# Kernel optimization log

Measured on AMD Instinct MI355X. Metric: run time of the kernel, lower is better.

The kernel has to match this reference:

```python
import jax, jax.numpy as jnp
import numpy as np

N, E, G = 20000, 320000, 64
IN, HID, HEADS, EDGE_D, ACT = 128, 256, 4, 5, 8
NEG_SLOPE = 0.2


def setup_inputs() -> dict:
    key = jax.random.key(0)
    ks = jax.random.split(key, 24)
    g = lambda i, shape, scale=0.05: jax.random.normal(ks[i], shape, dtype=jnp.float32) * scale
    inp = {
        "x": jax.random.normal(ks[0], (N, IN), dtype=jnp.float32),
        "edge_index": jax.random.randint(ks[1], (2, E), 0, N, dtype=jnp.int64),
        "batch": jnp.sort(jax.random.randint(ks[2], (N,), 0, G, dtype=jnp.int64)),
        "edge_attr": jax.random.normal(ks[3], (E, EDGE_D), dtype=jnp.float32),
        # GATv2 layer 1: in->64 per head, 4 heads, concat -> 256
        "W1l": g(4, (IN, HID)), "W1r": g(5, (IN, HID)), "W1e": g(6, (EDGE_D, HID)),
        "att1": g(7, (HEADS, HID // HEADS)), "b1": jnp.zeros((HID,), jnp.float32),
        # GATv2 layer 2: 256->256, 1 head
        "W2l": g(8, (HID, HID)), "W2r": g(9, (HID, HID)), "W2e": g(10, (EDGE_D, HID)),
        "att2": g(11, (1, HID)), "b2": jnp.zeros((HID,), jnp.float32),
        # heads
        "Wp": g(12, (HID, ACT)), "bp": jnp.zeros((ACT,), jnp.float32),
        "Wv": g(13, (HID, 1)), "bv": jnp.zeros((1,), jnp.float32),
    }
    return inp


def gatv2_conv(x, src, dst, edge_attr, Wl, Wr, We, att, bias, heads, concat):
    # PyG GATv2Conv (share_weights=False, add_self_loops=False):
    #   x_l = lin_l(x) (source msg), x_r = lin_r(x) (target), e = lin_edge(edge_attr)
    #   score = att . leaky_relu(x_l[src] + x_r[dst] + e); segment-softmax over dst
    #   out[i] = sum_j alpha_ij * x_l[j]
    n = x.shape[0]
    c = Wl.shape[1] // heads
    xl = (x @ Wl).reshape(n, heads, c)
    xr = (x @ Wr).reshape(n, heads, c)
    e = (edge_attr @ We).reshape(-1, heads, c)
    m = jax.nn.leaky_relu(xl[src] + xr[dst] + e, NEG_SLOPE)      # [E, H, C]
    logit = jnp.einsum("ehc,hc->eh", m, att)                      # [E, H]
    lmax = jax.ops.segment_max(logit, dst, num_segments=n)        # [N, H]
    unnorm = jnp.exp(logit - lmax[dst])
    denom = jax.ops.segment_sum(unnorm, dst, num_segments=n)
    alpha = unnorm / (denom[dst] + 1e-16)                         # [E, H]
    out = jax.ops.segment_sum(alpha[:, :, None] * xl[src], dst, num_segments=n)  # [N,H,C]
    out = out.reshape(n, heads * c) if concat else out.mean(axis=1)
    return out + bias


def reference(x, edge_index, batch, edge_attr,
              W1l, W1r, W1e, att1, b1,
              W2l, W2r, W2e, att2, b2,
              Wp, bp, Wv, bv):
    src, dst = edge_index[0], edge_index[1]
    h = gatv2_conv(x, src, dst, edge_attr, W1l, W1r, W1e, att1, b1, HEADS, True)
    h = jax.nn.relu(h)  # dropout p=0.0 -> identity
    h = gatv2_conv(h, src, dst, edge_attr, W2l, W2r, W2e, att2, b2, 1, False)
    h = jax.nn.relu(h)
    # global mean pool over graphs
    sums = jax.ops.segment_sum(h, batch, num_segments=G)
    cnt = jax.ops.segment_sum(jnp.ones((h.shape[0],), h.dtype), batch, num_segments=G)
    g = sums / jnp.maximum(cnt, 1.0)[:, None]
    logits = g @ Wp + bp                 # [G, ACT]
    value = (g @ Wv + bv)[:, 0]          # [G]
    # deterministic outputs (sampling excluded): concat logits and value
    return jnp.concatenate([logits, value[:, None]], axis=-1)  # [G, ACT+1]
```

## Files before the change

### kernel.cpp

```cpp
#include <hip/hip_runtime.h>
#include <math.h>

#define NN 20000
#define NE 320000
#define NG 64
#define IND 128
#define HIDD 256
#define NH 4
#define ED 5
#define NACT 8
#define NEG 0.2f
#define MAXDEG 64

__global__ __launch_bounds__(256) void gemm64(const float* __restrict__ A,
    const float* __restrict__ B, float* __restrict__ C, int M, int K, int Ncol)
{
    const int BK = 32;
    __shared__ float As[32][68];
    __shared__ float Bs[32][64];
    int bm = blockIdx.x * 64, bn = blockIdx.y * 64;
    int tid = threadIdx.x;
    int tx = tid & 15, ty = tid >> 4;
    float acc[4][4] = {};
    for (int k0 = 0; k0 < K; k0 += BK) {
        for (int idx = tid; idx < 64 * BK; idx += 256) {
            int r = idx >> 5, c = idx & 31;
            int gr = bm + r;
            As[c][r] = (gr < M) ? A[(size_t)gr * K + k0 + c] : 0.f;
        }
        for (int idx = tid; idx < BK * 64; idx += 256) {
            int r = idx >> 6, c = idx & 63;
            Bs[r][c] = B[(size_t)(k0 + r) * Ncol + bn + c];
        }
        __syncthreads();
        #pragma unroll
        for (int k = 0; k < BK; ++k) {
            float4 a4 = *(const float4*)&As[k][ty * 4];
            float4 b4 = *(const float4*)&Bs[k][tx * 4];
            float a[4] = {a4.x, a4.y, a4.z, a4.w};
            float b[4] = {b4.x, b4.y, b4.z, b4.w};
            #pragma unroll
            for (int i = 0; i < 4; ++i)
                #pragma unroll
                for (int j = 0; j < 4; ++j)
                    acc[i][j] = fmaf(a[i], b[j], acc[i][j]);
        }
        __syncthreads();
    }
    #pragma unroll
    for (int i = 0; i < 4; ++i) {
        int r = bm + ty * 4 + i;
        if (r < M) {
            float4 v = {acc[i][0], acc[i][1], acc[i][2], acc[i][3]};
            *(float4*)&C[(size_t)r * Ncol + bn + tx * 4] = v;
        }
    }
}

__global__ __launch_bounds__(256) void build_slots(const int* __restrict__ dst,
    int* __restrict__ deg, int* __restrict__ slots)
{
    int e = blockIdx.x * 256 + threadIdx.x;
    if (e >= NE) return;
    int d = dst[e];
    int pos = atomicAdd(&deg[d], 1);
    if (pos < MAXDEG) slots[d * MAXDEG + pos] = e;
}

template <int HEADS_T>
__global__ __launch_bounds__(256) void fused_agg(
    const int* __restrict__ deg, const int* __restrict__ slots,
    const int* __restrict__ src, const float* __restrict__ eattr,
    const float* __restrict__ xl, const float* __restrict__ xr,
    const float* __restrict__ We, const float* __restrict__ attw,
    const float* __restrict__ bias, float* __restrict__ out)
{
    __shared__ float sWe[ED * HIDD];
    __shared__ float sAtt[HIDD];
    for (int i = threadIdx.x; i < ED * HIDD; i += 256) sWe[i] = We[i];
    for (int i = threadIdx.x; i < HIDD; i += 256) sAtt[i] = attw[i];
    __syncthreads();

    int wave = threadIdx.x >> 6, lane = threadIdx.x & 63;
    int n = blockIdx.x * 4 + wave;
    int dg = min(deg[n], MAXDEG);
    int c0 = lane * 4;

    float attr_[4], wer[ED][4];
    #pragma unroll
    for (int j = 0; j < 4; ++j) attr_[j] = sAtt[c0 + j];
    #pragma unroll
    for (int k = 0; k < ED; ++k)
        #pragma unroll
        for (int j = 0; j < 4; ++j) wer[k][j] = sWe[k * HIDD + c0 + j];

    float4 xr4 = *(const float4*)(xr + (size_t)n * HIDD + c0);
    float xra[4] = {xr4.x, xr4.y, xr4.z, xr4.w};

    float denom = 0.f;
    float acc[4] = {0.f, 0.f, 0.f, 0.f};

    const int* slotrow = slots + (size_t)n * MAXDEG;
    for (int i = 0; i < dg; ++i) {
        int e = slotrow[i];
        int s = src[e];
        float4 xl4 = *(const float4*)(xl + (size_t)s * HIDD + c0);
        float xla[4] = {xl4.x, xl4.y, xl4.z, xl4.w};
        float ea[ED];
        #pragma unroll
        for (int k = 0; k < ED; ++k) ea[k] = eattr[(size_t)e * ED + k];
        float partial = 0.f;
        #pragma unroll
        for (int j = 0; j < 4; ++j) {
            float ev = 0.f;
            #pragma unroll
            for (int k = 0; k < ED; ++k) ev = fmaf(ea[k], wer[k][j], ev);
            float m = xla[j] + xra[j] + ev;
            m = m > 0.f ? m : NEG * m;
            partial = fmaf(m, attr_[j], partial);
        }
        if (HEADS_T == 4) {
            #pragma unroll
            for (int off = 1; off < 16; off <<= 1)
                partial += __shfl_xor(partial, off, 64);
        } else {
            #pragma unroll
            for (int off = 1; off < 64; off <<= 1)
                partial += __shfl_xor(partial, off, 64);
        }
        float ex = expf(partial);
        denom += ex;
        #pragma unroll
        for (int j = 0; j < 4; ++j) acc[j] = fmaf(ex, xla[j], acc[j]);
    }
    float inv = 1.f / (denom + 1e-16f);
    float4 o;
    o.x = fmaxf(acc[0] * inv + bias[c0 + 0], 0.f);
    o.y = fmaxf(acc[1] * inv + bias[c0 + 1], 0.f);
    o.z = fmaxf(acc[2] * inv + bias[c0 + 2], 0.f);
    o.w = fmaxf(acc[3] * inv + bias[c0 + 3], 0.f);
    *(float4*)(out + (size_t)n * HIDD + c0) = o;
}

#define POOL_CHUNK 128
__global__ __launch_bounds__(256) void pool_kernel(
    const float* __restrict__ h, const int* __restrict__ batch,
    float* __restrict__ pool, float* __restrict__ cnt)
{
    int c = threadIdx.x;
    int start = blockIdx.x * POOL_CHUNK;
    int end = min(start + POOL_CHUNK, NN);
    if (start >= NN) return;
    float acc = 0.f;
    int cur = batch[start];
    int localCount = 0;
    for (int n = start; n < end; ++n) {
        int g = batch[n];
        if (g != cur) {
            atomicAdd(&pool[cur * HIDD + c], acc);
            if (c == 0) atomicAdd(&cnt[cur], (float)localCount);
            acc = 0.f; localCount = 0; cur = g;
        }
        acc += h[(size_t)n * HIDD + c];
        ++localCount;
    }
    atomicAdd(&pool[cur * HIDD + c], acc);
    if (c == 0) atomicAdd(&cnt[cur], (float)localCount);
}

__global__ __launch_bounds__(256) void head_kernel(
    const float* __restrict__ pool, const float* __restrict__ cnt,
    const float* __restrict__ Wp, const float* __restrict__ bp,
    const float* __restrict__ Wv, const float* __restrict__ bv,
    float* __restrict__ out)
{
    int g = blockIdx.x;
    int c = threadIdx.x;
    float gv = pool[g * HIDD + c] / fmaxf(cnt[g], 1.0f);
    __shared__ float red[256];
    for (int j = 0; j < NACT + 1; ++j) {
        float w = (j < NACT) ? Wp[c * NACT + j] : Wv[c];
        red[c] = gv * w;
        __syncthreads();
        for (int sl = 128; sl > 0; sl >>= 1) {
            if (c < sl) red[c] += red[c + sl];
            __syncthreads();
        }
        if (c == 0) out[g * (NACT + 1) + j] = red[0] + ((j < NACT) ? bp[j] : bv[0]);
        __syncthreads();
    }
}

extern "C" void kernel_launch(void* const* d_in, const int* in_sizes, int n_in,
                              void* d_out, int out_size, void* d_ws, size_t ws_size,
                              hipStream_t stream)
{
    const float* x    = (const float*)d_in[0];
    const int*   ei   = (const int*)d_in[1];
    const int*   batch= (const int*)d_in[2];
    const float* ea   = (const float*)d_in[3];
    const float* W1l  = (const float*)d_in[4];
    const float* W1r  = (const float*)d_in[5];
    const float* W1e  = (const float*)d_in[6];
    const float* att1 = (const float*)d_in[7];
    const float* b1   = (const float*)d_in[8];
    const float* W2l  = (const float*)d_in[9];
    const float* W2r  = (const float*)d_in[10];
    const float* W2e  = (const float*)d_in[11];
    const float* att2 = (const float*)d_in[12];
    const float* b2   = (const float*)d_in[13];
    const float* Wp   = (const float*)d_in[14];
    const float* bp   = (const float*)d_in[15];
    const float* Wv   = (const float*)d_in[16];
    const float* bv   = (const float*)d_in[17];
    const int* src = ei;
    const int* dst = ei + NE;
    float* out = (float*)d_out;

    float* ws = (float*)d_ws;
    size_t off = 0;
    float* A     = ws + off; off += (size_t)NN * HIDD;
    float* B     = ws + off; off += (size_t)NN * HIDD;
    float* C     = ws + off; off += (size_t)NN * HIDD;
    float* D     = ws + off; off += (size_t)NN * HIDD;
    float* pool  = ws + off; off += (size_t)NG * HIDD;
    float* cnt   = ws + off; off += NG;
    int*   deg   = (int*)(ws + off); off += NN;
    int*   slots = (int*)(ws + off); off += (size_t)NN * MAXDEG;

    hipMemsetAsync(pool, 0, (size_t)(NG * HIDD + NG + NN) * sizeof(float), stream);

    build_slots<<<(NE + 255) / 256, 256, 0, stream>>>(dst, deg, slots);

    dim3 ggrid((NN + 63) / 64, HIDD / 64);
    gemm64<<<ggrid, 256, 0, stream>>>(x, W1l, A, NN, IND, HIDD);
    gemm64<<<ggrid, 256, 0, stream>>>(x, W1r, B, NN, IND, HIDD);
    fused_agg<4><<<NN / 4, 256, 0, stream>>>(deg, slots, src, ea, A, B, W1e, att1, b1, C);

    gemm64<<<ggrid, 256, 0, stream>>>(C, W2l, A, NN, HIDD, HIDD);
    gemm64<<<ggrid, 256, 0, stream>>>(C, W2r, B, NN, HIDD, HIDD);
    fused_agg<1><<<NN / 4, 256, 0, stream>>>(deg, slots, src, ea, A, B, W2e, att2, b2, D);

    pool_kernel<<<(NN + POOL_CHUNK - 1) / POOL_CHUNK, 256, 0, stream>>>(D, batch, pool, cnt);
    head_kernel<<<NG, 256, 0, stream>>>(pool, cnt, Wp, bp, Wv, bv, out);
}
```

Measured before the change: 485.0 us.

## Enlarge GEMM tile to 128x64, vectorize loads, and batch left/right projections

Replaces the 64x64-tile GEMM with a 128x64 tile where each thread computes an 8x4 output block, which raises arithmetic intensity per shared-memory load. Global loads of A and B now use float4. The two projections (Wl and Wr) run in one launch via blockIdx.z, removing one launch per layer. The trade-off is more registers per thread and a padded 129-wide As array, whose strided transposed writes may cause bank conflicts.

```diff
diff --git a/kernel.cpp b/kernel.cpp
--- a/kernel.cpp
+++ b/kernel.cpp
@@ -12,35 +12,51 @@
 #define NEG 0.2f
 #define MAXDEG 64
 
-__global__ __launch_bounds__(256) void gemm64(const float* __restrict__ A,
-    const float* __restrict__ B, float* __restrict__ C, int M, int K, int Ncol)
-{
-    const int BK = 32;
-    __shared__ float As[32][68];
+__global__ __launch_bounds__(256, 4) void gemm128x64(
+    const float* __restrict__ A, const float* __restrict__ Bl,
+    const float* __restrict__ Br, float* __restrict__ Cl, float* __restrict__ Cr,
+    int M, int K, int Ncol)
+{
+    const float* B = blockIdx.z ? Br : Bl;
+    float*       C = blockIdx.z ? Cr : Cl;
+    __shared__ float As[32][129];
     __shared__ float Bs[32][64];
-    int bm = blockIdx.x * 64, bn = blockIdx.y * 64;
+    int bm = blockIdx.x * 128, bn = blockIdx.y * 64;
     int tid = threadIdx.x;
     int tx = tid & 15, ty = tid >> 4;
-    float acc[4][4] = {};
-    for (int k0 = 0; k0 < K; k0 += BK) {
-        for (int idx = tid; idx < 64 * BK; idx += 256) {
-            int r = idx >> 5, c = idx & 31;
+    float acc[8][4] = {};
+    for (int k0 = 0; k0 < K; k0 += 32) {
+        #pragma unroll
+        for (int t = 0; t < 4; ++t) {
+            int idx = tid + t * 256;
+            int r = idx >> 3;
+            int c4 = (idx & 7) * 4;
             int gr = bm + r;
-            As[c][r] = (gr < M) ? A[(size_t)gr * K + k0 + c] : 0.f;
-        }
-        for (int idx = tid; idx < BK * 64; idx += 256) {
-            int r = idx >> 6, c = idx & 63;
-            Bs[r][c] = B[(size_t)(k0 + r) * Ncol + bn + c];
-        }
-        __syncthreads();
-        #pragma unroll
-        for (int k = 0; k < BK; ++k) {
-            float4 a4 = *(const float4*)&As[k][ty * 4];
-            float4 b4 = *(const float4*)&Bs[k][tx * 4];
-            float a[4] = {a4.x, a4.y, a4.z, a4.w};
-            float b[4] = {b4.x, b4.y, b4.z, b4.w};
-            #pragma unroll
-            for (int i = 0; i < 4; ++i)
+            float4 v = {0.f, 0.f, 0.f, 0.f};
+            if (gr < M) v = *(const float4*)&A[(size_t)gr * K + k0 + c4];
+            As[c4 + 0][r] = v.x;
+            As[c4 + 1][r] = v.y;
+            As[c4 + 2][r] = v.z;
+            As[c4 + 3][r] = v.w;
+        }
+        #pragma unroll
+        for (int t = 0; t < 2; ++t) {
+            int idx = tid + t * 256;
+            int r = idx >> 4;
+            int c4 = (idx & 15) * 4;
+            float4 v = *(const float4*)&B[(size_t)(k0 + r) * Ncol + bn + c4];
+            *(float4*)&Bs[r][c4] = v;
+        }
+        __syncthreads();
+        #pragma unroll
+        for (int k = 0; k < 32; ++k) {
+            float4 a0 = *(const float4*)&As[k][ty * 8];
+            float4 a1 = *(const float4*)&As[k][ty * 8 + 4];
+            float4 b0 = *(const float4*)&Bs[k][tx * 4];
+            float a[8] = {a0.x, a0.y, a0.z, a0.w, a1.x, a1.y, a1.z, a1.w};
+            float b[4] = {b0.x, b0.y, b0.z, b0.w};
+            #pragma unroll
+            for (int i = 0; i < 8; ++i)
                 #pragma unroll
                 for (int j = 0; j < 4; ++j)
                     acc[i][j] = fmaf(a[i], b[j], acc[i][j]);
@@ -48,8 +64,8 @@
         __syncthreads();
     }
     #pragma unroll
-    for (int i = 0; i < 4; ++i) {
-        int r = bm + ty * 4 + i;
+    for (int i = 0; i < 8; ++i) {
+        int r = bm + ty * 8 + i;
         if (r < M) {
             float4 v = {acc[i][0], acc[i][1], acc[i][2], acc[i][3]};
             *(float4*)&C[(size_t)r * Ncol + bn + tx * 4] = v;
@@ -232,13 +248,11 @@
 
     build_slots<<<(NE + 255) / 256, 256, 0, stream>>>(dst, deg, slots);
 
-    dim3 ggrid((NN + 63) / 64, HIDD / 64);
-    gemm64<<<ggrid, 256, 0, stream>>>(x, W1l, A, NN, IND, HIDD);
-    gemm64<<<ggrid, 256, 0, stream>>>(x, W1r, B, NN, IND, HIDD);
+    dim3 g1((NN + 127) / 128, HIDD / 64, 2);
+    gemm128x64<<<g1, 256, 0, stream>>>(x, W1l, W1r, A, B, NN, IND, HIDD);
     fused_agg<4><<<NN / 4, 256, 0, stream>>>(deg, slots, src, ea, A, B, W1e, att1, b1, C);
 
-    gemm64<<<ggrid, 256, 0, stream>>>(C, W2l, A, NN, HIDD, HIDD);
-    gemm64<<<ggrid, 256, 0, stream>>>(C, W2r, B, NN, HIDD, HIDD);
+    gemm128x64<<<g1, 256, 0, stream>>>(C, W2l, W2r, A, B, NN, HIDD, HIDD);
     fused_agg<1><<<NN / 4, 256, 0, stream>>>(deg, slots, src, ea, A, B, W2e, att2, b2, D);
 
     pool_kernel<<<(NN + POOL_CHUNK - 1) / POOL_CHUNK, 256, 0, stream>>>(D, batch, pool, cnt);
```

New measurement: 436.6 us. -10.0%, faster.
